# Kernel optimization log

Hardware: AMD Instinct MI355X
Metric: run time of the kernel (lower is better)

## Reference

```python
import jax, jax.numpy as jnp
import numpy as np

B, S, T = 32, 64, 64
E, H = 256, 512
VS, VT = 32000, 32000


def setup_inputs() -> dict:
    key = jax.random.key(0)
    ks = jax.random.split(key, 32)
    g = lambda i, shape: jax.random.normal(ks[i], shape, jnp.float32) * 0.05
    inp = {
        "src": jax.random.randint(ks[0], (B, S), 0, VS),
        "tgt": jax.random.randint(ks[1], (B, T), 0, VT),
        # encoder
        "enc_emb": g(2, (VS, E)),
        "enc_wih0": g(3, (3 * H, E)), "enc_whh0": g(4, (3 * H, H)),
        "enc_bih0": g(5, (3 * H,)), "enc_bhh0": g(6, (3 * H,)),
        "enc_wih1": g(7, (3 * H, H)), "enc_whh1": g(8, (3 * H, H)),
        "enc_bih1": g(9, (3 * H,)), "enc_bhh1": g(10, (3 * H,)),
        # decoder (layer0 input = embed + encoder context = E + H)
        "dec_emb": g(11, (VT, E)),
        "dec_wih0": g(12, (3 * H, E + H)), "dec_whh0": g(13, (3 * H, H)),
        "dec_bih0": g(14, (3 * H,)), "dec_bhh0": g(15, (3 * H,)),
        "dec_wih1": g(16, (3 * H, H)), "dec_whh1": g(17, (3 * H, H)),
        "dec_bih1": g(18, (3 * H,)), "dec_bhh1": g(19, (3 * H,)),
        # general (Luong) attention: score = q W_a k^T
        "attn_w": g(20, (H, H)),
        # output projection: Linear(hidden + enc_hidden -> tgt_vocab)
        "out_w": g(21, (VT, 2 * H)), "out_b": g(22, (VT,)),
    }
    return inp


def _gru_step(x, h, wih, whh, bih, bhh):
    # torch GRU cell math
    gi = x @ wih.T + bih
    gh = h @ whh.T + bhh
    i_r, i_z, i_n = jnp.split(gi, 3, axis=-1)
    h_r, h_z, h_n = jnp.split(gh, 3, axis=-1)
    r = jax.nn.sigmoid(i_r + h_r)
    z = jax.nn.sigmoid(i_z + h_z)
    n = jnp.tanh(i_n + r * h_n)
    return (1.0 - z) * n + z * h


def reference(src, tgt, enc_emb, enc_wih0, enc_whh0, enc_bih0, enc_bhh0,
              enc_wih1, enc_whh1, enc_bih1, enc_bhh1,
              dec_emb, dec_wih0, dec_whh0, dec_bih0, dec_bhh0,
              dec_wih1, dec_whh1, dec_bih1, dec_bhh1,
              attn_w, out_w, out_b):
    b = src.shape[0]
    h = enc_whh0.shape[1]
    # ---- encoder: 2-layer GRU over src ----
    xs = jnp.swapaxes(enc_emb[src], 0, 1)  # [S, B, E]
    h0 = jnp.zeros((b, h), jnp.float32)
    h1 = jnp.zeros((b, h), jnp.float32)

    def enc_step(carry, x_t):
        c0, c1 = carry
        c0 = _gru_step(x_t, c0, enc_wih0, enc_whh0, enc_bih0, enc_bhh0)
        c1 = _gru_step(c0, c1, enc_wih1, enc_whh1, enc_bih1, enc_bhh1)
        return (c0, c1), c1

    (h0, h1), enc_seq = jax.lax.scan(enc_step, (h0, h1), xs)
    enc_out = jnp.swapaxes(enc_seq, 0, 1)  # [B, S, H]
    mask = src == 0  # pad positions

    # ---- decoder: teacher forcing (ratio=1.0) over tgt[:, :-1] ----
    ctx0 = jnp.zeros((b, h), jnp.float32)
    toks = jnp.swapaxes(tgt[:, :-1], 0, 1)  # [T-1, B]

    def dec_step(carry, tok):
        d0, d1, ctx = carry
        emb = dec_emb[tok]  # [B, E]
        rin = jnp.concatenate([emb, ctx], axis=-1)
        d0 = _gru_step(rin, d0, dec_wih0, dec_whh0, dec_bih0, dec_bhh0)
        d1 = _gru_step(d0, d1, dec_wih1, dec_whh1, dec_bih1, dec_bhh1)
        # general attention: score = (q W_a) . k
        scores = jnp.einsum('bh,hk,bsk->bs', d1, attn_w, enc_out)
        scores = jnp.where(mask, -1e9, scores)
        w = jax.nn.softmax(scores, axis=-1)
        new_ctx = jnp.einsum('bs,bsh->bh', w, enc_out)
        logits = jnp.concatenate([d1, new_ctx], axis=-1) @ out_w.T + out_b
        return (d0, d1, new_ctx), logits

    _, logits = jax.lax.scan(dec_step, (h0, h1, ctx0), toks)
    return jnp.swapaxes(logits, 0, 1)  # [B, T-1, VT]
```

## Files before the change

kernel.cpp:

```cpp
#include <hip/hip_runtime.h>

#define Bz   32
#define Sz   64
#define Tdec 63
#define Ez   256
#define Hz   512
#define H3z  1536
#define Vz   32000
#define NB   128

typedef __attribute__((ext_vector_type(4))) float f32x4;
typedef __attribute__((ext_vector_type(4))) float floatx4;
typedef __attribute__((ext_vector_type(8))) short shortx8;
typedef __attribute__((ext_vector_type(8))) unsigned short u16x8;

__device__ __forceinline__ unsigned short f2bf(float f) {
  unsigned x = __float_as_uint(f);
  unsigned r = (x + 0x7fffu + ((x >> 16) & 1u)) >> 16;
  return (unsigned short)r;
}

__device__ __forceinline__ f32x4 ld_sc_nw(const f32x4* p) {
  f32x4 r;
  asm volatile("global_load_dwordx4 %0, %1, off sc0 sc1" : "=&v"(r) : "v"(p));
  return r;
}
__device__ __forceinline__ void wait_vm0() {
  asm volatile("s_waitcnt vmcnt(0)" ::: "memory");
}
__device__ __forceinline__ void ld2f_sc(const float* p0, const float* p1,
                                        float& a, float& b) {
  asm volatile(
      "global_load_dword %0, %2, off sc0 sc1\n\t"
      "global_load_dword %1, %3, off sc0 sc1\n\t"
      "s_waitcnt vmcnt(0)"
      : "=&v"(a), "=&v"(b) : "v"(p0), "v"(p1) : "memory");
}
__device__ __forceinline__ void st_sc(float* p, float v) {
  asm volatile("global_store_dword %0, %1, off sc0 sc1" :: "v"(p), "v"(v) : "memory");
}
__device__ __forceinline__ void st_flag(unsigned* p, unsigned v) {
  asm volatile("global_store_dword %0, %1, off sc0 sc1" :: "v"(p), "v"(v) : "memory");
}
__device__ __forceinline__ void ld2u_sc(const unsigned* p0, const unsigned* p1,
                                        unsigned& a, unsigned& b) {
  asm volatile(
      "global_load_dword %0, %2, off sc0 sc1\n\t"
      "global_load_dword %1, %3, off sc0 sc1\n\t"
      "s_waitcnt vmcnt(0)"
      : "=&v"(a), "=&v"(b) : "v"(p0), "v"(p1) : "memory");
}

__global__ __launch_bounds__(256)
void k_transpose(const float* __restrict__ in, int R, int Ctot, int c0,
                 float* __restrict__ out) {
  __shared__ float tile[32][33];
  int ct = blockIdx.x * 32;
  int rt = blockIdx.y * 32;
  int lx = threadIdx.x & 31, ly = threadIdx.x >> 5;
#pragma unroll
  for (int i = 0; i < 32; i += 8)
    tile[ly + i][lx] = in[(long)(rt + ly + i) * Ctot + c0 + ct + lx];
  __syncthreads();
#pragma unroll
  for (int i = 0; i < 32; i += 8)
    out[(long)(ct + ly + i) * R + rt + lx] = tile[lx][ly + i];
}

__global__ __launch_bounds__(256)
void k_pack4(const float* __restrict__ in, int rs, int c0,
             float* __restrict__ out, int k4off) {
  int jl = threadIdx.x & 15, k4l = threadIdx.x >> 4;
  int j = blockIdx.y * 16 + jl;
  int k4 = blockIdx.x * 16 + k4l;
  float4 v = *(const float4*)(in + (long)j * rs + c0 + k4 * 4);
  *(float4*)(out + ((long)(k4 + k4off) * H3z + j) * 4) = v;
}

__global__ __launch_bounds__(256)
void k_packbf(const float* __restrict__ in, int rs, int c0,
              unsigned short* __restrict__ out, int k8off) {
  int jl = threadIdx.x & 31, k8l = threadIdx.x >> 5;
  int j = blockIdx.y * 32 + jl;
  int k8 = blockIdx.x * 8 + k8l;
  const float* src = in + (long)j * rs + c0 + k8 * 8;
  float4 a = *(const float4*)src;
  float4 b = *(const float4*)(src + 4);
  u16x8 o;
  o[0] = f2bf(a.x); o[1] = f2bf(a.y); o[2] = f2bf(a.z); o[3] = f2bf(a.w);
  o[4] = f2bf(b.x); o[5] = f2bf(b.y); o[6] = f2bf(b.z); o[7] = f2bf(b.w);
  *(u16x8*)(out + ((long)(k8 + k8off) * H3z + j) * 8) = o;
}

__global__ __launch_bounds__(256)
void k_embed_gi(const int* __restrict__ toks, const float* __restrict__ emb,
                const float* __restrict__ W4, const float* __restrict__ bias,
                float* __restrict__ G) {
  __shared__ float se[16][Ez];
  int jg = blockIdx.x % 24;
  int rg = blockIdx.x / 24;
  int r0 = rg * 16;
  int tid = threadIdx.x;
  for (int c = tid; c < 16 * Ez; c += 256) {
    int rl = c >> 8;
    int k = c & 255;
    int r = r0 + rl;
    int tok = toks[(r & 31) * 64 + (r >> 5)];
    se[rl][k] = emb[(long)tok * Ez + k];
  }
  __syncthreads();
  int jj = tid & 63, rq = tid >> 6;
  int j = jg * 64 + jj;
  float a0 = 0.f, a1 = 0.f, a2 = 0.f, a3 = 0.f;
#pragma unroll 4
  for (int k4 = 0; k4 < 64; ++k4) {
    float4 w = *(const float4*)(W4 + ((long)k4 * H3z + j) * 4);
    const float* s0 = &se[rq * 4 + 0][k4 * 4];
    const float* s1 = &se[rq * 4 + 1][k4 * 4];
    const float* s2 = &se[rq * 4 + 2][k4 * 4];
    const float* s3 = &se[rq * 4 + 3][k4 * 4];
    a0 = fmaf(s0[3], w.w, fmaf(s0[2], w.z, fmaf(s0[1], w.y, fmaf(s0[0], w.x, a0))));
    a1 = fmaf(s1[3], w.w, fmaf(s1[2], w.z, fmaf(s1[1], w.y, fmaf(s1[0], w.x, a1))));
    a2 = fmaf(s2[3], w.w, fmaf(s2[2], w.z, fmaf(s2[1], w.y, fmaf(s2[0], w.x, a2))));
    a3 = fmaf(s3[3], w.w, fmaf(s3[2], w.z, fmaf(s3[1], w.y, fmaf(s3[0], w.x, a3))));
  }
  float bj = bias[j];
  G[(long)(r0 + rq * 4 + 0) * H3z + j] = a0 + bj;
  G[(long)(r0 + rq * 4 + 1) * H3z + j] = a1 + bj;
  G[(long)(r0 + rq * 4 + 2) * H3z + j] = a2 + bj;
  G[(long)(r0 + rq * 4 + 3) * H3z + j] = a3 + bj;
}

__global__ void k_f2bf(const float* __restrict__ in, unsigned short* __restrict__ out, long n4) {
  long i = (long)blockIdx.x * blockDim.x + threadIdx.x;
  long stride = (long)gridDim.x * blockDim.x;
  for (; i < n4; i += stride) {
    float4 v = ((const float4*)in)[i];
    ushort4 o;
    o.x = f2bf(v.x); o.y = f2bf(v.y); o.z = f2bf(v.z); o.w = f2bf(v.w);
    ((ushort4*)out)[i] = o;
  }
}

struct PP {
  const float* giEnc;
  const float* giDec;
  const unsigned short* W8e0;
  const unsigned short* W8e1;
  const unsigned short* W8d0;
  const unsigned short* W8d1;
  const float* enc_bhh0;
  const float* enc_bih1;
  const float* enc_bhh1;
  const float* dec_bhh0;
  const float* dec_bih1;
  const float* dec_bhh1;
  const float* wtAttn;
  const int* src;
  float* h0; float* h1; float* d0; float* d1; float* ctx;
  float* encOut;
  float* encN;
  float* keN;
  unsigned* flags;
  unsigned short* d1ctxBf;
};

__device__ __forceinline__ void gsync(unsigned* flags, unsigned ph) {
  wait_vm0();
  __syncthreads();
  int tid = threadIdx.x;
  if (tid == 0) st_flag(&flags[blockIdx.x], ph);
  if (tid < 64) {
    const unsigned* p0 = &flags[tid];
    const unsigned* p1 = &flags[tid + 64];
    for (;;) {
      unsigned f0, f1;
      ld2u_sc(p0, p1, f0, f1);
      if (!__any(f0 < ph || f1 < ph)) break;
      __builtin_amdgcn_s_sleep(1);
    }
  }
  __syncthreads();
}

template <int HASX>
__device__ __forceinline__ void gru_cell(
    int blkid, const unsigned short* __restrict__ W8,
    const float* __restrict__ gi, const float* __restrict__ bih,
    const float* __restrict__ bhh,
    const float* __restrict__ xin, const float* __restrict__ hin,
    float* __restrict__ hout, float* __restrict__ fout, long fstride,
    unsigned short* __restrict__ bfout, float* smem) {
  float* sh = smem;
  float* sx = smem + 2048;
  float* part = smem + 4096;
  const int jg = blkid & 7, bg = blkid >> 3;
  const int tid = threadIdx.x;
  const int l = tid & 63;
  const int kq = tid >> 6;
  const int j = jg * 64 + l;
  constexpr int Q8 = HASX ? 32 : 16;
  constexpr int G8 = Q8 / 2;
  const u16x8* Wr0 = (const u16x8*)W8 + (long)(kq * Q8) * H3z + j;

  u16x8 wA[2][3], wB[2][3];
  {
    const u16x8* Wr = Wr0;
    wA[0][0] = Wr[0];    wA[0][1] = Wr[512];  wA[0][2] = Wr[1024];
    wA[1][0] = Wr[1536]; wA[1][1] = Wr[2048]; wA[1][2] = Wr[2560];
  }
  float gir = 0.f, giz = 0.f, gin = 0.f;
  {
    const int b4 = tid >> 6, jc = tid & 63;
    const int b = bg * 4 + b4, jj = jg * 64 + jc;
    if (gi) {
      gir = gi[(long)b * H3z + jj];
      giz = gi[(long)b * H3z + 512 + jj];
      gin = gi[(long)b * H3z + 1024 + jj];
    }
    if (bih) { gir += bih[jj]; giz += bih[512 + jj]; gin += bih[1024 + jj]; }
  }
  {
    const f32x4* hp = (const f32x4*)(hin + bg * 2048);
    if (HASX) {
      const f32x4* xp = (const f32x4*)(xin + bg * 2048);
      f32x4 a = ld_sc_nw(hp + tid);
      f32x4 b = ld_sc_nw(hp + tid + 256);
      f32x4 c = ld_sc_nw(xp + tid);
      f32x4 d = ld_sc_nw(xp + tid + 256);
      wait_vm0();
      ((f32x4*)sh)[tid] = a; ((f32x4*)sh)[tid + 256] = b;
      ((f32x4*)sx)[tid] = c; ((f32x4*)sx)[tid + 256] = d;
    } else {
      f32x4 a = ld_sc_nw(hp + tid);
      f32x4 b = ld_sc_nw(hp + tid + 256);
      wait_vm0();
      ((f32x4*)sh)[tid] = a; ((f32x4*)sh)[tid + 256] = b;
    }
  }
  __syncthreads();

  const float* vb;
  if (HASX) vb = (kq < 2) ? (sx + kq * 256) : (sh + (kq - 2) * 256);
  else      vb = sh + kq * 128;
  float pr[4] = {0, 0, 0, 0}, pz[4] = {0, 0, 0, 0}, pn[4] = {0, 0, 0, 0};

  auto loadg = [&](u16x8 (&w)[2][3], int g) {
    const u16x8* Wr = Wr0 + (long)(2 * g) * H3z;
    w[0][0] = Wr[0];    w[0][1] = Wr[512];  w[0][2] = Wr[1024];
    w[1][0] = Wr[1536]; w[1][1] = Wr[2048]; w[1][2] = Wr[2560];
  };
  auto compg = [&](u16x8 (&w)[2][3], int g) {
#pragma unroll
    for (int r = 0; r < 2; ++r) {
      const int kk = 2 * g + r;
      float f0[8], f1[8], f2[8];
#pragma unroll
      for (int e = 0; e < 8; ++e) {
        f0[e] = __uint_as_float((unsigned)w[r][0][e] << 16);
        f1[e] = __uint_as_float((unsigned)w[r][1][e] << 16);
        f2[e] = __uint_as_float((unsigned)w[r][2][e] << 16);
      }
#pragma unroll
      for (int b4 = 0; b4 < 4; ++b4) {
        const float* v = vb + kk * 8 + b4 * 512;
        f32x4 v0 = *(const f32x4*)v;
        f32x4 v1 = *(const f32x4*)(v + 4);
#pragma unroll
        for (int e = 0; e < 4; ++e) {
          pr[b4] = fmaf(v0[e], f0[e], pr[b4]);
          pz[b4] = fmaf(v0[e], f1[e], pz[b4]);
          pn[b4] = fmaf(v0[e], f2[e], pn[b4]);
        }
#pragma unroll
        for (int e = 0; e < 4; ++e) {
          pr[b4] = fmaf(v1[e], f0[4 + e], pr[b4]);
          pz[b4] = fmaf(v1[e], f1[4 + e], pz[b4]);
          pn[b4] = fmaf(v1[e], f2[4 + e], pn[b4]);
        }
      }
    }
  };
#pragma unroll
  for (int g = 0; g < G8; g += 2) {
    if (g + 1 < G8) loadg(wB, g + 1);
    compg(wA, g);
    if (g + 2 < G8) loadg(wA, g + 2);
    if (g + 1 < G8) compg(wB, g + 1);
  }

#pragma unroll
  for (int b4 = 0; b4 < 4; ++b4) {
    part[((0 * 4 + b4) * 4 + kq) * 64 + l] = pr[b4];
    part[((1 * 4 + b4) * 4 + kq) * 64 + l] = pz[b4];
    part[((2 * 4 + b4) * 4 + kq) * 64 + l] = pn[b4];
  }
  __syncthreads();
  {
    const int b4 = tid >> 6, jc = tid & 63;
    const int b = bg * 4 + b4;
    const int jj = jg * 64 + jc;
    float sr = 0.f, sz = 0.f, snx = 0.f, snh = 0.f;
#pragma unroll
    for (int q = 0; q < 4; ++q) {
      sr += part[((0 * 4 + b4) * 4 + q) * 64 + jc];
      sz += part[((1 * 4 + b4) * 4 + q) * 64 + jc];
      float pnq = part[((2 * 4 + b4) * 4 + q) * 64 + jc];
      if (HASX && q < 2) snx += pnq; else snh += pnq;
    }
    float rv = 1.f / (1.f + __expf(-(gir + sr + bhh[jj])));
    float zv = 1.f / (1.f + __expf(-(giz + sz + bhh[512 + jj])));
    float nv = tanhf(gin + snx + rv * (snh + bhh[1024 + jj]));
    float hv = sh[b4 * 512 + jj];
    float hp = (1.f - zv) * nv + zv * hv;
    st_sc(hout + (long)b * 512 + jj, hp);
    if (fout) st_sc(fout + (long)b * fstride + jj, hp);
    if (bfout) bfout[(long)b * 1024 + jj] = f2bf(hp);
  }
}

__device__ void ke_phase(int blk, const float* __restrict__ encOut,
                         const float* __restrict__ attn_wT,
                         float* __restrict__ keN, float* __restrict__ encN,
                         float* smem) {
  int b = blk & 31, sq = blk >> 5;
  long r0 = (long)b * 64 + sq * 16;
  int tid = threadIdx.x;
  {
    const f32x4* ep = (const f32x4*)(encOut + r0 * 512);
    f32x4 v[8];
#pragma unroll
    for (int u = 0; u < 8; ++u) v[u] = ld_sc_nw(ep + tid + u * 256);
    wait_vm0();
    f32x4* en = (f32x4*)(encN + r0 * 512);
#pragma unroll
    for (int u = 0; u < 8; ++u) {
      ((f32x4*)smem)[tid + u * 256] = v[u];
      en[tid + u * 256] = v[u];
    }
  }
  __syncthreads();
  int jj = tid & 63, rq = tid >> 6;
  float acc[4][8];
#pragma unroll
  for (int r = 0; r < 4; ++r)
#pragma unroll
    for (int jc = 0; jc < 8; ++jc) acc[r][jc] = 0.f;
#pragma unroll 2
  for (int k = 0; k < 512; ++k) {
    float w[8];
#pragma unroll
    for (int jc = 0; jc < 8; ++jc) w[jc] = attn_wT[(long)k * 512 + jc * 64 + jj];
#pragma unroll
    for (int r = 0; r < 4; ++r) {
      float e = smem[(rq * 4 + r) * 512 + k];
#pragma unroll
      for (int jc = 0; jc < 8; ++jc) acc[r][jc] = fmaf(e, w[jc], acc[r][jc]);
    }
  }
#pragma unroll
  for (int r = 0; r < 4; ++r)
#pragma unroll
    for (int jc = 0; jc < 8; ++jc)
      keN[(r0 + rq * 4 + r) * 512 + jc * 64 + jj] = acc[r][jc];
}

__device__ void attn_phase(int b, const float* __restrict__ d1,
                           const float* __restrict__ keN,
                           const float* __restrict__ encN,
                           const int* __restrict__ src,
                           float* __restrict__ ctxn,
                           unsigned short* __restrict__ bfctx, float* smem) {
  float* sd = smem;
  float* sc = smem + 512;
  int tid = threadIdx.x;
  {
    float a, c;
    ld2f_sc(d1 + b * 512 + tid, d1 + b * 512 + tid + 256, a, c);
    sd[tid] = a;
    sd[tid + 256] = c;
  }
  __syncthreads();
  int s = tid >> 2, q = tid & 3;
  const float4* kp = (const float4*)(keN + ((long)b * 64 + s) * 512 + q * 128);
  const float4* dp = (const float4*)(sd + q * 128);
  float p = 0.f;
#pragma unroll 8
  for (int i = 0; i < 32; ++i) {
    float4 v = kp[i];
    float4 d = dp[i];
    p += v.x * d.x + v.y * d.y + v.z * d.z + v.w * d.w;
  }
  p += __shfl_xor(p, 1);
  p += __shfl_xor(p, 2);
  if (q == 0) sc[s] = (src[b * 64 + s] == 0) ? -1e9f : p;
  __syncthreads();
  if (tid < 64) {
    float v = sc[tid];
    float m = v;
    for (int o = 32; o; o >>= 1) m = fmaxf(m, __shfl_xor(m, o));
    float e = __expf(v - m);
    float sum = e;
    for (int o = 32; o; o >>= 1) sum += __shfl_xor(sum, o);
    sc[tid] = e / sum;
  }
  __syncthreads();
  float a0 = 0.f, a1 = 0.f;
#pragma unroll 4
  for (int s2 = 0; s2 < 64; ++s2) {
    float w = sc[s2];
    const float* er = encN + ((long)b * 64 + s2) * 512;
    a0 = fmaf(w, er[tid], a0);
    a1 = fmaf(w, er[tid + 256], a1);
  }
  st_sc(ctxn + b * 512 + tid, a0);
  st_sc(ctxn + b * 512 + tid + 256, a1);
  bfctx[b * 1024 + tid] = f2bf(a0);
  bfctx[b * 1024 + tid + 256] = f2bf(a1);
}

__global__ __launch_bounds__(256) void k_persist(PP P) {
  __shared__ float smem[8192];
  int blk = blockIdx.x;
  unsigned ph = 0;
  for (int i = 0; i < Sz + 1; ++i) {
    if (i < Sz && blk < 64) {
      gru_cell<0>(blk, P.W8e0, P.giEnc + (long)i * 49152, nullptr, P.enc_bhh0,
                  nullptr, P.h0 + (i & 1) * 16384, P.h0 + ((i + 1) & 1) * 16384,
                  nullptr, 0, nullptr, smem);
    } else if (i >= 1 && blk >= 64) {
      int t = i - 1;
      gru_cell<1>(blk - 64, P.W8e1, nullptr, P.enc_bih1, P.enc_bhh1,
                  P.h0 + (i & 1) * 16384, P.h1 + (t & 1) * 16384,
                  P.h1 + ((t + 1) & 1) * 16384,
                  P.encOut + (long)t * 512, (long)Sz * 512, nullptr, smem);
    }
    gsync(P.flags, ++ph);
  }
  ke_phase(blk, P.encOut, P.wtAttn, P.keN, P.encN, smem);
  gsync(P.flags, ++ph);
  for (int t = 0; t < Tdec; ++t) {
    int cs = t & 1, ns = (t + 1) & 1;
    const float* d0in = (t == 0) ? P.h0 : P.d0 + cs * 16384;
    const float* d1in = (t == 0) ? P.h1 : P.d1 + cs * 16384;
    if (blk < 64) {
      gru_cell<1>(blk, P.W8d0, P.giDec + (long)t * 49152, nullptr, P.dec_bhh0,
                  P.ctx + cs * 16384, d0in, P.d0 + ns * 16384,
                  nullptr, 0, nullptr, smem);
    }
    gsync(P.flags, ++ph);
    if (blk < 64) {
      gru_cell<1>(blk, P.W8d1, nullptr, P.dec_bih1, P.dec_bhh1,
                  P.d0 + ns * 16384, d1in, P.d1 + ns * 16384,
                  nullptr, 0, P.d1ctxBf + (long)t * 32768, smem);
    }
    gsync(P.flags, ++ph);
    if (blk < 32) {
      attn_phase(blk, P.d1 + ns * 16384, P.keN, P.encN, P.src,
                 P.ctx + ns * 16384, P.d1ctxBf + (long)t * 32768 + 512, smem);
    }
    gsync(P.flags, ++ph);
  }
}

__global__ __launch_bounds__(256)
void k_out_gemm(const unsigned short* __restrict__ A, const unsigned short* __restrict__ Bw,
                const float* __restrict__ bias, float* __restrict__ out) {
  __shared__ __align__(16) char lds[32768];
  int bid = blockIdx.x;
  int bm = bid & 15, bn = bid >> 4;
  long m0 = (long)bm * 128, n0 = (long)bn * 128;
  int tid = threadIdx.x, lane = tid & 63, wid = tid >> 6;
  int wm = wid >> 1, wn = wid & 1;
  floatx4 acc[4][4];
#pragma unroll
  for (int i = 0; i < 4; i++)
#pragma unroll
    for (int jx = 0; jx < 4; jx++) acc[i][jx] = (floatx4){0.f, 0.f, 0.f, 0.f};

  int rl = lane >> 3;
  int kb = (((lane & 7) ^ rl) << 4);

  for (int kt = 0; kt < 16; ++kt) {
    long kbyte0 = (long)kt * 128;
#pragma unroll
    for (int q = 0; q < 4; ++q) {
      int c = wid * 4 + q;
      int row = c * 8 + rl;
      const char* ga = (const char*)A + (m0 + row) * 2048 + kbyte0 + kb;
      const char* gb = (const char*)Bw + (n0 + row) * 2048 + kbyte0 + kb;
      __builtin_amdgcn_global_load_lds(
          (const __attribute__((address_space(1))) void*)ga,
          (__attribute__((address_space(3))) void*)(lds + (c << 10)), 16, 0, 0);
      __builtin_amdgcn_global_load_lds(
          (const __attribute__((address_space(1))) void*)gb,
          (__attribute__((address_space(3))) void*)(lds + 16384 + (c << 10)), 16, 0, 0);
    }
    asm volatile("s_waitcnt vmcnt(0)" ::: "memory");
    __syncthreads();
#pragma unroll
    for (int kk = 0; kk < 2; ++kk) {
      shortx8 af[4], bf[4];
#pragma unroll
      for (int f = 0; f < 4; ++f) {
        int rowA = wm * 64 + f * 16 + (lane & 15);
        int cbA = (kk * 64 + ((lane >> 4) << 4)) ^ ((rowA & 7) << 4);
        af[f] = *(const shortx8*)(lds + rowA * 128 + cbA);
        int rowB = wn * 64 + f * 16 + (lane & 15);
        int cbB = (kk * 64 + ((lane >> 4) << 4)) ^ ((rowB & 7) << 4);
        bf[f] = *(const shortx8*)(lds + 16384 + rowB * 128 + cbB);
      }
#pragma unroll
      for (int mf = 0; mf < 4; ++mf)
#pragma unroll
        for (int nf = 0; nf < 4; ++nf)
          acc[mf][nf] = __builtin_amdgcn_mfma_f32_16x16x32_bf16(af[mf], bf[nf], acc[mf][nf], 0, 0, 0);
    }
    __syncthreads();
  }
#pragma unroll
  for (int mf = 0; mf < 4; ++mf) {
#pragma unroll
    for (int nf = 0; nf < 4; ++nf) {
      long gn = n0 + wn * 64 + nf * 16 + (lane & 15);
      float bb = bias[gn];
#pragma unroll
      for (int r = 0; r < 4; ++r) {
        long gm = m0 + wm * 64 + mf * 16 + ((lane >> 4) * 4) + r;
        if (gm < (long)Tdec * Bz) {
          long t = gm >> 5, b = gm & 31;
          out[(b * Tdec + t) * (long)Vz + gn] = acc[mf][nf][r] + bb;
        }
      }
    }
  }
}

extern "C" void kernel_launch(void* const* d_in, const int* in_sizes, int n_in,
                              void* d_out, int out_size, void* d_ws, size_t ws_size,
                              hipStream_t stream) {
  const int*   src      = (const int*)d_in[0];
  const int*   tgt      = (const int*)d_in[1];
  const float* enc_emb  = (const float*)d_in[2];
  const float* enc_wih0 = (const float*)d_in[3];
  const float* enc_whh0 = (const float*)d_in[4];
  const float* enc_bih0 = (const float*)d_in[5];
  const float* enc_bhh0 = (const float*)d_in[6];
  const float* enc_wih1 = (const float*)d_in[7];
  const float* enc_whh1 = (const float*)d_in[8];
  const float* enc_bih1 = (const float*)d_in[9];
  const float* enc_bhh1 = (const float*)d_in[10];
  const float* dec_emb  = (const float*)d_in[11];
  const float* dec_wih0 = (const float*)d_in[12];
  const float* dec_whh0 = (const float*)d_in[13];
  const float* dec_bih0 = (const float*)d_in[14];
  const float* dec_bhh0 = (const float*)d_in[15];
  const float* dec_wih1 = (const float*)d_in[16];
  const float* dec_whh1 = (const float*)d_in[17];
  const float* dec_bih1 = (const float*)d_in[18];
  const float* dec_bhh1 = (const float*)d_in[19];
  const float* attn_w   = (const float*)d_in[20];
  const float* out_w    = (const float*)d_in[21];
  const float* out_b    = (const float*)d_in[22];
  float* out = (float*)d_out;

  char* ws = (char*)d_ws;
  size_t off = 0;
  auto alloc = [&](size_t bytes) -> char* {
    char* p = ws + off;
    off += (bytes + 255) & ~(size_t)255;
    return p;
  };
  float* W4embE = (float*)alloc((size_t)Ez * H3z * 4);
  float* W4embD = (float*)alloc((size_t)Ez * H3z * 4);
  unsigned short* W8e0 = (unsigned short*)alloc((size_t)64 * H3z * 8 * 2);
  unsigned short* W8e1 = (unsigned short*)alloc((size_t)128 * H3z * 8 * 2);
  unsigned short* W8d0 = (unsigned short*)alloc((size_t)128 * H3z * 8 * 2);
  unsigned short* W8d1 = (unsigned short*)alloc((size_t)128 * H3z * 8 * 2);
  float* wtAttn = (float*)alloc((size_t)Hz * Hz * 4);
  float* giEnc  = (float*)alloc((size_t)Sz * Bz * H3z * 4);
  float* giDec  = (float*)alloc((size_t)Tdec * Bz * H3z * 4);
  float* encOut = (float*)alloc((size_t)Bz * Sz * Hz * 4);
  float* encN   = (float*)alloc((size_t)Bz * Sz * Hz * 4);
  float* keN    = (float*)alloc((size_t)Bz * Sz * Hz * 4);
  float* h0buf  = (float*)alloc((size_t)2 * Bz * Hz * 4);
  float* h1buf  = (float*)alloc((size_t)2 * Bz * Hz * 4);
  float* d0buf  = (float*)alloc((size_t)2 * Bz * Hz * 4);
  float* d1buf  = (float*)alloc((size_t)2 * Bz * Hz * 4);
  float* ctxbuf = (float*)alloc((size_t)2 * Bz * Hz * 4);
  unsigned short* d1ctxBf = (unsigned short*)alloc((size_t)2048 * 1024 * 2);
  unsigned short* outwBf  = (unsigned short*)alloc((size_t)Vz * 1024 * 2);
  unsigned* flags = (unsigned*)alloc(NB * 4);
  if (off > ws_size) return;

  dim3 tb(256);
  k_pack4<<<dim3(4, 96), tb, 0, stream>>>(enc_wih0, Ez, 0, W4embE, 0);
  k_pack4<<<dim3(4, 96), tb, 0, stream>>>(dec_wih0, Ez + Hz, 0, W4embD, 0);
  k_packbf<<<dim3(8, 48), tb, 0, stream>>>(enc_whh0, Hz, 0, W8e0, 0);
  k_packbf<<<dim3(8, 48), tb, 0, stream>>>(enc_wih1, Hz, 0, W8e1, 0);
  k_packbf<<<dim3(8, 48), tb, 0, stream>>>(enc_whh1, Hz, 0, W8e1, 64);
  k_packbf<<<dim3(8, 48), tb, 0, stream>>>(dec_wih0, Ez + Hz, Ez, W8d0, 0);
  k_packbf<<<dim3(8, 48), tb, 0, stream>>>(dec_whh0, Hz, 0, W8d0, 64);
  k_packbf<<<dim3(8, 48), tb, 0, stream>>>(dec_wih1, Hz, 0, W8d1, 0);
  k_packbf<<<dim3(8, 48), tb, 0, stream>>>(dec_whh1, Hz, 0, W8d1, 64);
  k_transpose<<<dim3(Hz / 32, Hz / 32), tb, 0, stream>>>(attn_w, Hz, Hz, 0, wtAttn);

  hipMemsetAsync(h0buf, 0, (size_t)2 * Bz * Hz * 4, stream);
  hipMemsetAsync(h1buf, 0, (size_t)2 * Bz * Hz * 4, stream);
  hipMemsetAsync(ctxbuf, 0, (size_t)2 * Bz * Hz * 4, stream);
  hipMemsetAsync(d1ctxBf + (size_t)2016 * 1024, 0, (size_t)32 * 1024 * 2, stream);
  hipMemsetAsync(flags, 0, NB * 4, stream);

  k_embed_gi<<<24 * 128, tb, 0, stream>>>(src, enc_emb, W4embE, enc_bih0, giEnc);
  k_embed_gi<<<24 * 126, tb, 0, stream>>>(tgt, dec_emb, W4embD, dec_bih0, giDec);
  k_f2bf<<<2048, tb, 0, stream>>>(out_w, outwBf, (long)Vz * 1024 / 4);

  PP pp;
  pp.giEnc = giEnc; pp.giDec = giDec;
  pp.W8e0 = W8e0; pp.W8e1 = W8e1; pp.W8d0 = W8d0; pp.W8d1 = W8d1;
  pp.enc_bhh0 = enc_bhh0; pp.enc_bih1 = enc_bih1; pp.enc_bhh1 = enc_bhh1;
  pp.dec_bhh0 = dec_bhh0; pp.dec_bih1 = dec_bih1; pp.dec_bhh1 = dec_bhh1;
  pp.wtAttn = wtAttn; pp.src = src;
  pp.h0 = h0buf; pp.h1 = h1buf; pp.d0 = d0buf; pp.d1 = d1buf; pp.ctx = ctxbuf;
  pp.encOut = encOut; pp.encN = encN; pp.keN = keN;
  pp.d1ctxBf = d1ctxBf; pp.flags = flags;
  k_persist<<<NB, tb, 0, stream>>>(pp);

  k_out_gemm<<<16 * 250, tb, 0, stream>>>(d1ctxBf, outwBf, out_b, out);
}
```

Baseline: 4.639 ms.

## Split decoder GRU into x/h parts across block halves, widen to 512 threads

```diff
diff --git a/kernel.cpp b/kernel.cpp
--- a/kernel.cpp
+++ b/kernel.cpp
@@ -19,6 +19,9 @@
   unsigned r = (x + 0x7fffu + ((x >> 16) & 1u)) >> 16;
   return (unsigned short)r;
 }
+__device__ __forceinline__ float bf2f(unsigned short u) {
+  return __uint_as_float((unsigned)u << 16);
+}
 
 __device__ __forceinline__ f32x4 ld_sc_nw(const f32x4* p) {
   f32x4 r;
@@ -28,13 +31,23 @@
 __device__ __forceinline__ void wait_vm0() {
   asm volatile("s_waitcnt vmcnt(0)" ::: "memory");
 }
-__device__ __forceinline__ void ld2f_sc(const float* p0, const float* p1,
-                                        float& a, float& b) {
+__device__ __forceinline__ void ld1f_sc(const float* p, float& a) {
   asm volatile(
-      "global_load_dword %0, %2, off sc0 sc1\n\t"
-      "global_load_dword %1, %3, off sc0 sc1\n\t"
+      "global_load_dword %0, %1, off sc0 sc1\n\t"
       "s_waitcnt vmcnt(0)"
-      : "=&v"(a), "=&v"(b) : "v"(p0), "v"(p1) : "memory");
+      : "=&v"(a) : "v"(p) : "memory");
+}
+__device__ __forceinline__ void ld4f_sc(const float* p0, const float* p1,
+                                        const float* p2, const float* p3,
+                                        float& a, float& b, float& c, float& d) {
+  asm volatile(
+      "global_load_dword %0, %4, off sc0 sc1\n\t"
+      "global_load_dword %1, %5, off sc0 sc1\n\t"
+      "global_load_dword %2, %6, off sc0 sc1\n\t"
+      "global_load_dword %3, %7, off sc0 sc1\n\t"
+      "s_waitcnt vmcnt(0)"
+      : "=&v"(a), "=&v"(b), "=&v"(c), "=&v"(d)
+      : "v"(p0), "v"(p1), "v"(p2), "v"(p3) : "memory");
 }
 __device__ __forceinline__ void st_sc(float* p, float v) {
   asm volatile("global_store_dword %0, %1, off sc0 sc1" :: "v"(p), "v"(v) : "memory");
@@ -147,8 +160,10 @@
   const float* giDec;
   const unsigned short* W8e0;
   const unsigned short* W8e1;
-  const unsigned short* W8d0;
-  const unsigned short* W8d1;
+  const unsigned short* W8d0x;
+  const unsigned short* W8d0h;
+  const unsigned short* W8d1x;
+  const unsigned short* W8d1h;
   const float* enc_bhh0;
   const float* enc_bih1;
   const float* enc_bhh1;
@@ -158,9 +173,10 @@
   const float* wtAttn;
   const int* src;
   float* h0; float* h1; float* d0; float* d1; float* ctx;
+  float* hpd0; float* hpd1;
   float* encOut;
-  float* encN;
-  float* keN;
+  unsigned short* keNb;
+  unsigned short* encNb;
   unsigned* flags;
   unsigned short* d1ctxBf;
 };
@@ -183,34 +199,34 @@
   __syncthreads();
 }
 
+#define W_PREFETCH_G0(Wr0, wA)                                        \
+  { const u16x8* Wr = (Wr0);                                          \
+    wA[0][0] = Wr[0];    wA[0][1] = Wr[512];  wA[0][2] = Wr[1024];    \
+    wA[1][0] = Wr[1536]; wA[1][1] = Wr[2048]; wA[1][2] = Wr[2560]; }
+
 template <int HASX>
-__device__ __forceinline__ void gru_cell(
+__device__ __forceinline__ void gru_full(
     int blkid, const unsigned short* __restrict__ W8,
     const float* __restrict__ gi, const float* __restrict__ bih,
     const float* __restrict__ bhh,
     const float* __restrict__ xin, const float* __restrict__ hin,
     float* __restrict__ hout, float* __restrict__ fout, long fstride,
-    unsigned short* __restrict__ bfout, float* smem) {
+    float* smem) {
   float* sh = smem;
   float* sx = smem + 2048;
   float* part = smem + 4096;
   const int jg = blkid & 7, bg = blkid >> 3;
   const int tid = threadIdx.x;
-  const int l = tid & 63;
-  const int kq = tid >> 6;
+  const int l = tid & 63, kq = tid >> 6;
   const int j = jg * 64 + l;
-  constexpr int Q8 = HASX ? 32 : 16;
+  constexpr int Q8 = HASX ? 16 : 8;
   constexpr int G8 = Q8 / 2;
   const u16x8* Wr0 = (const u16x8*)W8 + (long)(kq * Q8) * H3z + j;
 
   u16x8 wA[2][3], wB[2][3];
-  {
-    const u16x8* Wr = Wr0;
-    wA[0][0] = Wr[0];    wA[0][1] = Wr[512];  wA[0][2] = Wr[1024];
-    wA[1][0] = Wr[1536]; wA[1][1] = Wr[2048]; wA[1][2] = Wr[2560];
-  }
+  W_PREFETCH_G0(Wr0, wA);
   float gir = 0.f, giz = 0.f, gin = 0.f;
-  {
+  if (tid < 256) {
     const int b4 = tid >> 6, jc = tid & 63;
     const int b = bg * 4 + b4, jj = jg * 64 + jc;
     if (gi) {
@@ -222,29 +238,23 @@
   }
   {
     const f32x4* hp = (const f32x4*)(hin + bg * 2048);
+    f32x4 a = ld_sc_nw(hp + tid);
     if (HASX) {
       const f32x4* xp = (const f32x4*)(xin + bg * 2048);
-      f32x4 a = ld_sc_nw(hp + tid);
-      f32x4 b = ld_sc_nw(hp + tid + 256);
       f32x4 c = ld_sc_nw(xp + tid);
-      f32x4 d = ld_sc_nw(xp + tid + 256);
       wait_vm0();
-      ((f32x4*)sh)[tid] = a; ((f32x4*)sh)[tid + 256] = b;
-      ((f32x4*)sx)[tid] = c; ((f32x4*)sx)[tid + 256] = d;
+      ((f32x4*)sh)[tid] = a;
+      ((f32x4*)sx)[tid] = c;
     } else {
-      f32x4 a = ld_sc_nw(hp + tid);
-      f32x4 b = ld_sc_nw(hp + tid + 256);
       wait_vm0();
-      ((f32x4*)sh)[tid] = a; ((f32x4*)sh)[tid + 256] = b;
-    }
-  }
-  __syncthreads();
-
+      ((f32x4*)sh)[tid] = a;
+    }
+  }
+  __syncthreads();
   const float* vb;
-  if (HASX) vb = (kq < 2) ? (sx + kq * 256) : (sh + (kq - 2) * 256);
-  else      vb = sh + kq * 128;
+  if (HASX) vb = (kq < 4) ? (sx + kq * 128) : (sh + (kq - 4) * 128);
+  else      vb = sh + kq * 64;
   float pr[4] = {0, 0, 0, 0}, pz[4] = {0, 0, 0, 0}, pn[4] = {0, 0, 0, 0};
-
   auto loadg = [&](u16x8 (&w)[2][3], int g) {
     const u16x8* Wr = Wr0 + (long)(2 * g) * H3z;
     w[0][0] = Wr[0];    w[0][1] = Wr[512];  w[0][2] = Wr[1024];
@@ -257,9 +267,7 @@
       float f0[8], f1[8], f2[8];
 #pragma unroll
       for (int e = 0; e < 8; ++e) {
-        f0[e] = __uint_as_float((unsigned)w[r][0][e] << 16);
-        f1[e] = __uint_as_float((unsigned)w[r][1][e] << 16);
-        f2[e] = __uint_as_float((unsigned)w[r][2][e] << 16);
+        f0[e] = bf2f(w[r][0][e]); f1[e] = bf2f(w[r][1][e]); f2[e] = bf2f(w[r][2][e]);
       }
 #pragma unroll
       for (int b4 = 0; b4 < 4; ++b4) {
@@ -288,62 +296,258 @@
     if (g + 2 < G8) loadg(wA, g + 2);
     if (g + 1 < G8) compg(wB, g + 1);
   }
-
 #pragma unroll
   for (int b4 = 0; b4 < 4; ++b4) {
-    part[((0 * 4 + b4) * 4 + kq) * 64 + l] = pr[b4];
-    part[((1 * 4 + b4) * 4 + kq) * 64 + l] = pz[b4];
-    part[((2 * 4 + b4) * 4 + kq) * 64 + l] = pn[b4];
-  }
-  __syncthreads();
-  {
+    part[((0 * 4 + b4) * 8 + kq) * 64 + l] = pr[b4];
+    part[((1 * 4 + b4) * 8 + kq) * 64 + l] = pz[b4];
+    part[((2 * 4 + b4) * 8 + kq) * 64 + l] = pn[b4];
+  }
+  __syncthreads();
+  if (tid < 256) {
     const int b4 = tid >> 6, jc = tid & 63;
     const int b = bg * 4 + b4;
     const int jj = jg * 64 + jc;
     float sr = 0.f, sz = 0.f, snx = 0.f, snh = 0.f;
 #pragma unroll
-    for (int q = 0; q < 4; ++q) {
-      sr += part[((0 * 4 + b4) * 4 + q) * 64 + jc];
-      sz += part[((1 * 4 + b4) * 4 + q) * 64 + jc];
-      float pnq = part[((2 * 4 + b4) * 4 + q) * 64 + jc];
-      if (HASX && q < 2) snx += pnq; else snh += pnq;
+    for (int q = 0; q < 8; ++q) {
+      sr += part[((0 * 4 + b4) * 8 + q) * 64 + jc];
+      sz += part[((1 * 4 + b4) * 8 + q) * 64 + jc];
+      float pnq = part[((2 * 4 + b4) * 8 + q) * 64 + jc];
+      if (HASX && q < 4) snx += pnq; else snh += pnq;
     }
     float rv = 1.f / (1.f + __expf(-(gir + sr + bhh[jj])));
     float zv = 1.f / (1.f + __expf(-(giz + sz + bhh[512 + jj])));
     float nv = tanhf(gin + snx + rv * (snh + bhh[1024 + jj]));
     float hv = sh[b4 * 512 + jj];
-    float hp = (1.f - zv) * nv + zv * hv;
-    st_sc(hout + (long)b * 512 + jj, hp);
-    if (fout) st_sc(fout + (long)b * fstride + jj, hp);
-    if (bfout) bfout[(long)b * 1024 + jj] = f2bf(hp);
+    float hp2 = (1.f - zv) * nv + zv * hv;
+    st_sc(hout + (long)b * 512 + jj, hp2);
+    if (fout) st_sc(fout + (long)b * fstride + jj, hp2);
+  }
+}
+
+__device__ __forceinline__ void gru_xpart(
+    int blkid, const unsigned short* __restrict__ Wx,
+    const float* __restrict__ gi, const float* __restrict__ bih,
+    const float* __restrict__ bhh,
+    const float* __restrict__ xin, const float* __restrict__ hprev,
+    const float* __restrict__ hp, float* __restrict__ hout,
+    unsigned short* __restrict__ bfout, float* smem) {
+  float* sx = smem;
+  float* part = smem + 4096;
+  const int jg = blkid & 7, bg = blkid >> 3;
+  const int tid = threadIdx.x;
+  const int l = tid & 63, kq = tid >> 6;
+  const int j = jg * 64 + l;
+  const u16x8* Wr0 = (const u16x8*)Wx + (long)(kq * 8) * H3z + j;
+  u16x8 wA[2][3], wB[2][3];
+  W_PREFETCH_G0(Wr0, wA);
+  float gir = 0.f, giz = 0.f, gin = 0.f;
+  if (tid < 256) {
+    const int b4 = tid >> 6, jc = tid & 63;
+    const int b = bg * 4 + b4, jj = jg * 64 + jc;
+    if (gi) {
+      gir = gi[(long)b * H3z + jj];
+      giz = gi[(long)b * H3z + 512 + jj];
+      gin = gi[(long)b * H3z + 1024 + jj];
+    }
+    if (bih) { gir += bih[jj]; giz += bih[512 + jj]; gin += bih[1024 + jj]; }
+  }
+  {
+    const f32x4* xp = (const f32x4*)(xin + bg * 2048);
+    f32x4 a = ld_sc_nw(xp + tid);
+    wait_vm0();
+    ((f32x4*)sx)[tid] = a;
+  }
+  __syncthreads();
+  const float* vb = sx + kq * 64;
+  float pr[4] = {0, 0, 0, 0}, pz[4] = {0, 0, 0, 0}, pn[4] = {0, 0, 0, 0};
+  auto loadg = [&](u16x8 (&w)[2][3], int g) {
+    const u16x8* Wr = Wr0 + (long)(2 * g) * H3z;
+    w[0][0] = Wr[0];    w[0][1] = Wr[512];  w[0][2] = Wr[1024];
+    w[1][0] = Wr[1536]; w[1][1] = Wr[2048]; w[1][2] = Wr[2560];
+  };
+  auto compg = [&](u16x8 (&w)[2][3], int g) {
+#pragma unroll
+    for (int r = 0; r < 2; ++r) {
+      const int kk = 2 * g + r;
+      float f0[8], f1[8], f2[8];
+#pragma unroll
+      for (int e = 0; e < 8; ++e) {
+        f0[e] = bf2f(w[r][0][e]); f1[e] = bf2f(w[r][1][e]); f2[e] = bf2f(w[r][2][e]);
+      }
+#pragma unroll
+      for (int b4 = 0; b4 < 4; ++b4) {
+        const float* v = vb + kk * 8 + b4 * 512;
+        f32x4 v0 = *(const f32x4*)v;
+        f32x4 v1 = *(const f32x4*)(v + 4);
+#pragma unroll
+        for (int e = 0; e < 4; ++e) {
+          pr[b4] = fmaf(v0[e], f0[e], pr[b4]);
+          pz[b4] = fmaf(v0[e], f1[e], pz[b4]);
+          pn[b4] = fmaf(v0[e], f2[e], pn[b4]);
+        }
+#pragma unroll
+        for (int e = 0; e < 4; ++e) {
+          pr[b4] = fmaf(v1[e], f0[4 + e], pr[b4]);
+          pz[b4] = fmaf(v1[e], f1[4 + e], pz[b4]);
+          pn[b4] = fmaf(v1[e], f2[4 + e], pn[b4]);
+        }
+      }
+    }
+  };
+#pragma unroll
+  for (int g = 0; g < 4; g += 2) {
+    loadg(wB, g + 1);
+    compg(wA, g);
+    if (g + 2 < 4) loadg(wA, g + 2);
+    compg(wB, g + 1);
+  }
+#pragma unroll
+  for (int b4 = 0; b4 < 4; ++b4) {
+    part[((0 * 4 + b4) * 8 + kq) * 64 + l] = pr[b4];
+    part[((1 * 4 + b4) * 8 + kq) * 64 + l] = pz[b4];
+    part[((2 * 4 + b4) * 8 + kq) * 64 + l] = pn[b4];
+  }
+  __syncthreads();
+  if (tid < 256) {
+    const int b4 = tid >> 6, jc = tid & 63;
+    const int b = bg * 4 + b4;
+    const int jj = jg * 64 + jc;
+    float hr, hz, hn, hv;
+    ld4f_sc(hp + (long)(0 * 32 + b) * 512 + jj, hp + (long)(1 * 32 + b) * 512 + jj,
+            hp + (long)(2 * 32 + b) * 512 + jj, hprev + (long)b * 512 + jj,
+            hr, hz, hn, hv);
+    float sr = 0.f, sz = 0.f, sn = 0.f;
+#pragma unroll
+    for (int q = 0; q < 8; ++q) {
+      sr += part[((0 * 4 + b4) * 8 + q) * 64 + jc];
+      sz += part[((1 * 4 + b4) * 8 + q) * 64 + jc];
+      sn += part[((2 * 4 + b4) * 8 + q) * 64 + jc];
+    }
+    float rv = 1.f / (1.f + __expf(-(gir + sr + hr + bhh[jj])));
+    float zv = 1.f / (1.f + __expf(-(giz + sz + hz + bhh[512 + jj])));
+    float nv = tanhf(gin + sn + rv * (hn + bhh[1024 + jj]));
+    float hp2 = (1.f - zv) * nv + zv * hv;
+    st_sc(hout + (long)b * 512 + jj, hp2);
+    if (bfout) bfout[(long)b * 1024 + jj] = f2bf(hp2);
+  }
+}
+
+__device__ __forceinline__ void gru_hpart(
+    int blkid, const unsigned short* __restrict__ Wh,
+    const float* __restrict__ hin, float* __restrict__ hpOut, float* smem) {
+  float* sh = smem;
+  float* part = smem + 4096;
+  const int jg = blkid & 7, bg = blkid >> 3;
+  const int tid = threadIdx.x;
+  const int l = tid & 63, kq = tid >> 6;
+  const int j = jg * 64 + l;
+  const u16x8* Wr0 = (const u16x8*)Wh + (long)(kq * 8) * H3z + j;
+  u16x8 wA[2][3], wB[2][3];
+  W_PREFETCH_G0(Wr0, wA);
+  {
+    const f32x4* hp = (const f32x4*)(hin + bg * 2048);
+    f32x4 a = ld_sc_nw(hp + tid);
+    wait_vm0();
+    ((f32x4*)sh)[tid] = a;
+  }
+  __syncthreads();
+  const float* vb = sh + kq * 64;
+  float pr[4] = {0, 0, 0, 0}, pz[4] = {0, 0, 0, 0}, pn[4] = {0, 0, 0, 0};
+  auto loadg = [&](u16x8 (&w)[2][3], int g) {
+    const u16x8* Wr = Wr0 + (long)(2 * g) * H3z;
+    w[0][0] = Wr[0];    w[0][1] = Wr[512];  w[0][2] = Wr[1024];
+    w[1][0] = Wr[1536]; w[1][1] = Wr[2048]; w[1][2] = Wr[2560];
+  };
+  auto compg = [&](u16x8 (&w)[2][3], int g) {
+#pragma unroll
+    for (int r = 0; r < 2; ++r) {
+      const int kk = 2 * g + r;
+      float f0[8], f1[8], f2[8];
+#pragma unroll
+      for (int e = 0; e < 8; ++e) {
+        f0[e] = bf2f(w[r][0][e]); f1[e] = bf2f(w[r][1][e]); f2[e] = bf2f(w[r][2][e]);
+      }
+#pragma unroll
+      for (int b4 = 0; b4 < 4; ++b4) {
+        const float* v = vb + kk * 8 + b4 * 512;
+        f32x4 v0 = *(const f32x4*)v;
+        f32x4 v1 = *(const f32x4*)(v + 4);
+#pragma unroll
+        for (int e = 0; e < 4; ++e) {
+          pr[b4] = fmaf(v0[e], f0[e], pr[b4]);
+          pz[b4] = fmaf(v0[e], f1[e], pz[b4]);
+          pn[b4] = fmaf(v0[e], f2[e], pn[b4]);
+        }
+#pragma unroll
+        for (int e = 0; e < 4; ++e) {
+          pr[b4] = fmaf(v1[e], f0[4 + e], pr[b4]);
+          pz[b4] = fmaf(v1[e], f1[4 + e], pz[b4]);
+          pn[b4] = fmaf(v1[e], f2[4 + e], pn[b4]);
+        }
+      }
+    }
+  };
+#pragma unroll
+  for (int g = 0; g < 4; g += 2) {
+    loadg(wB, g + 1);
+    compg(wA, g);
+    if (g + 2 < 4) loadg(wA, g + 2);
+    compg(wB, g + 1);
+  }
+#pragma unroll
+  for (int b4 = 0; b4 < 4; ++b4) {
+    part[((0 * 4 + b4) * 8 + kq) * 64 + l] = pr[b4];
+    part[((1 * 4 + b4) * 8 + kq) * 64 + l] = pz[b4];
+    part[((2 * 4 + b4) * 8 + kq) * 64 + l] = pn[b4];
+  }
+  __syncthreads();
+  if (tid < 256) {
+    const int b4 = tid >> 6, jc = tid & 63;
+    const int b = bg * 4 + b4;
+    const int jj = jg * 64 + jc;
+    float s0 = 0.f, s1 = 0.f, s2 = 0.f;
+#pragma unroll
+    for (int q = 0; q < 8; ++q) {
+      s0 += part[((0 * 4 + b4) * 8 + q) * 64 + jc];
+      s1 += part[((1 * 4 + b4) * 8 + q) * 64 + jc];
+      s2 += part[((2 * 4 + b4) * 8 + q) * 64 + jc];
+    }
+    st_sc(hpOut + (long)(0 * 32 + b) * 512 + jj, s0);
+    st_sc(hpOut + (long)(1 * 32 + b) * 512 + jj, s1);
+    st_sc(hpOut + (long)(2 * 32 + b) * 512 + jj, s2);
   }
 }
 
 __device__ void ke_phase(int blk, const float* __restrict__ encOut,
                          const float* __restrict__ attn_wT,
-                         float* __restrict__ keN, float* __restrict__ encN,
-                         float* smem) {
+                         unsigned short* __restrict__ keNb,
+                         unsigned short* __restrict__ encNb, float* smem) {
   int b = blk & 31, sq = blk >> 5;
   long r0 = (long)b * 64 + sq * 16;
   int tid = threadIdx.x;
   {
     const f32x4* ep = (const f32x4*)(encOut + r0 * 512);
-    f32x4 v[8];
-#pragma unroll
-    for (int u = 0; u < 8; ++u) v[u] = ld_sc_nw(ep + tid + u * 256);
+    f32x4 v[4];
+#pragma unroll
+    for (int u = 0; u < 4; ++u) v[u] = ld_sc_nw(ep + tid + u * 512);
     wait_vm0();
-    f32x4* en = (f32x4*)(encN + r0 * 512);
-#pragma unroll
-    for (int u = 0; u < 8; ++u) {
-      ((f32x4*)smem)[tid + u * 256] = v[u];
-      en[tid + u * 256] = v[u];
-    }
-  }
-  __syncthreads();
+#pragma unroll
+    for (int u = 0; u < 4; ++u) ((f32x4*)smem)[tid + u * 512] = v[u];
+  }
+  __syncthreads();
+  {
+    u16x8 o0, o1;
+    const float* s = smem + tid * 16;
+#pragma unroll
+    for (int e = 0; e < 8; ++e) { o0[e] = f2bf(s[e]); o1[e] = f2bf(s[8 + e]); }
+    *(u16x8*)(encNb + r0 * 512 + tid * 16) = o0;
+    *(u16x8*)(encNb + r0 * 512 + tid * 16 + 8) = o1;
+  }
   int jj = tid & 63, rq = tid >> 6;
-  float acc[4][8];
-#pragma unroll
-  for (int r = 0; r < 4; ++r)
+  float acc[2][8];
+#pragma unroll
+  for (int r = 0; r < 2; ++r)
 #pragma unroll
     for (int jc = 0; jc < 8; ++jc) acc[r][jc] = 0.f;
 #pragma unroll 2
@@ -351,23 +555,23 @@
     float w[8];
 #pragma unroll
     for (int jc = 0; jc < 8; ++jc) w[jc] = attn_wT[(long)k * 512 + jc * 64 + jj];
-#pragma unroll
-    for (int r = 0; r < 4; ++r) {
-      float e = smem[(rq * 4 + r) * 512 + k];
-#pragma unroll
-      for (int jc = 0; jc < 8; ++jc) acc[r][jc] = fmaf(e, w[jc], acc[r][jc]);
-    }
-  }
-#pragma unroll
-  for (int r = 0; r < 4; ++r)
+    float e0 = smem[(rq * 2) * 512 + k], e1 = smem[(rq * 2 + 1) * 512 + k];
+#pragma unroll
+    for (int jc = 0; jc < 8; ++jc) {
+      acc[0][jc] = fmaf(e0, w[jc], acc[0][jc]);
+      acc[1][jc] = fmaf(e1, w[jc], acc[1][jc]);
+    }
+  }
+#pragma unroll
+  for (int r = 0; r < 2; ++r)
 #pragma unroll
     for (int jc = 0; jc < 8; ++jc)
-      keN[(r0 + rq * 4 + r) * 512 + jc * 64 + jj] = acc[r][jc];
+      keNb[(r0 + rq * 2 + r) * 512 + jc * 64 + jj] = f2bf(acc[r][jc]);
 }
 
 __device__ void attn_phase(int b, const float* __restrict__ d1,
-                           const float* __restrict__ keN,
-                           const float* __restrict__ encN,
+                           const unsigned short* __restrict__ keNb,
+                           const unsigned short* __restrict__ encNb,
                            const int* __restrict__ src,
                            float* __restrict__ ctxn,
                            unsigned short* __restrict__ bfctx, float* smem) {
@@ -375,24 +579,24 @@
   float* sc = smem + 512;
   int tid = threadIdx.x;
   {
-    float a, c;
-    ld2f_sc(d1 + b * 512 + tid, d1 + b * 512 + tid + 256, a, c);
+    float a;
+    ld1f_sc(d1 + b * 512 + tid, a);
     sd[tid] = a;
-    sd[tid + 256] = c;
-  }
-  __syncthreads();
-  int s = tid >> 2, q = tid & 3;
-  const float4* kp = (const float4*)(keN + ((long)b * 64 + s) * 512 + q * 128);
-  const float4* dp = (const float4*)(sd + q * 128);
+  }
+  __syncthreads();
+  int s = tid >> 3, q = tid & 7;
+  const u16x8* kp = (const u16x8*)(keNb + ((long)b * 64 + s) * 512 + q * 64);
+  const float* dp = sd + q * 64;
   float p = 0.f;
-#pragma unroll 8
-  for (int i = 0; i < 32; ++i) {
-    float4 v = kp[i];
-    float4 d = dp[i];
-    p += v.x * d.x + v.y * d.y + v.z * d.z + v.w * d.w;
+#pragma unroll
+  for (int e = 0; e < 8; ++e) {
+    u16x8 kv = kp[e];
+#pragma unroll
+    for (int i = 0; i < 8; ++i) p = fmaf(bf2f(kv[i]), dp[e * 8 + i], p);
   }
   p += __shfl_xor(p, 1);
   p += __shfl_xor(p, 2);
+  p += __shfl_xor(p, 4);
   if (q == 0) sc[s] = (src[b * 64 + s] == 0) ? -1e9f : p;
   __syncthreads();
   if (tid < 64) {
@@ -405,60 +609,58 @@
     sc[tid] = e / sum;
   }
   __syncthreads();
-  float a0 = 0.f, a1 = 0.f;
-#pragma unroll 4
-  for (int s2 = 0; s2 < 64; ++s2) {
-    float w = sc[s2];
-    const float* er = encN + ((long)b * 64 + s2) * 512;
-    a0 = fmaf(w, er[tid], a0);
-    a1 = fmaf(w, er[tid + 256], a1);
-  }
+  float a0 = 0.f;
+  const unsigned short* er = encNb + (long)b * 64 * 512 + tid;
+#pragma unroll 8
+  for (int s2 = 0; s2 < 64; ++s2) a0 = fmaf(sc[s2], bf2f(er[(long)s2 * 512]), a0);
   st_sc(ctxn + b * 512 + tid, a0);
-  st_sc(ctxn + b * 512 + tid + 256, a1);
   bfctx[b * 1024 + tid] = f2bf(a0);
-  bfctx[b * 1024 + tid + 256] = f2bf(a1);
-}
-
-__global__ __launch_bounds__(256) void k_persist(PP P) {
-  __shared__ float smem[8192];
+}
+
+__global__ __launch_bounds__(512, 2) void k_persist(PP P) {
+  __shared__ float smem[10240];
   int blk = blockIdx.x;
   unsigned ph = 0;
   for (int i = 0; i < Sz + 1; ++i) {
-    if (i < Sz && blk < 64) {
-      gru_cell<0>(blk, P.W8e0, P.giEnc + (long)i * 49152, nullptr, P.enc_bhh0,
-                  nullptr, P.h0 + (i & 1) * 16384, P.h0 + ((i + 1) & 1) * 16384,
-                  nullptr, 0, nullptr, smem);
-    } else if (i >= 1 && blk >= 64) {
+    if (blk < 64) {
+      if (i < Sz)
+        gru_full<0>(blk, P.W8e0, P.giEnc + (long)i * 49152, nullptr, P.enc_bhh0,
+                    nullptr, P.h0 + (i & 1) * 16384, P.h0 + ((i + 1) & 1) * 16384,
+                    nullptr, 0, smem);
+    } else if (i >= 1) {
       int t = i - 1;
-      gru_cell<1>(blk - 64, P.W8e1, nullptr, P.enc_bih1, P.enc_bhh1,
+      gru_full<1>(blk - 64, P.W8e1, nullptr, P.enc_bih1, P.enc_bhh1,
                   P.h0 + (i & 1) * 16384, P.h1 + (t & 1) * 16384,
                   P.h1 + ((t + 1) & 1) * 16384,
-                  P.encOut + (long)t * 512, (long)Sz * 512, nullptr, smem);
+                  P.encOut + (long)t * 512, (long)Sz * 512, smem);
     }
     gsync(P.flags, ++ph);
   }
-  ke_phase(blk, P.encOut, P.wtAttn, P.keN, P.encN, smem);
+  ke_phase(blk, P.encOut, P.wtAttn, P.keNb, P.encNb, smem);
+  gsync(P.flags, ++ph);
+  if (blk < 64) gru_hpart(blk, P.W8d0h, P.h0, P.hpd0, smem);
   gsync(P.flags, ++ph);
   for (int t = 0; t < Tdec; ++t) {
-    int cs = t & 1, ns = (t + 1) & 1;
-    const float* d0in = (t == 0) ? P.h0 : P.d0 + cs * 16384;
-    const float* d1in = (t == 0) ? P.h1 : P.d1 + cs * 16384;
-    if (blk < 64) {
-      gru_cell<1>(blk, P.W8d0, P.giDec + (long)t * 49152, nullptr, P.dec_bhh0,
-                  P.ctx + cs * 16384, d0in, P.d0 + ns * 16384,
-                  nullptr, 0, nullptr, smem);
-    }
+    int cs = t & 1, ps = cs ^ 1;
+    const float* d0prev = (t == 0) ? P.h0 : P.d0 + ps * 16384;
+    const float* d1prev = (t == 0) ? P.h1 : P.d1 + ps * 16384;
+    if (blk < 64)
+      gru_xpart(blk, P.W8d0x, P.giDec + (long)t * 49152, nullptr, P.dec_bhh0,
+                P.ctx + ps * 16384, d0prev, P.hpd0 + cs * 49152,
+                P.d0 + cs * 16384, nullptr, smem);
+    else
+      gru_hpart(blk - 64, P.W8d1h, d1prev, P.hpd1 + cs * 49152, smem);
     gsync(P.flags, ++ph);
-    if (blk < 64) {
-      gru_cell<1>(blk, P.W8d1, nullptr, P.dec_bih1, P.dec_bhh1,
-                  P.d0 + ns * 16384, d1in, P.d1 + ns * 16384,
-                  nullptr, 0, P.d1ctxBf + (long)t * 32768, smem);
-    }
+    if (blk < 64)
+      gru_xpart(blk, P.W8d1x, nullptr, P.dec_bih1, P.dec_bhh1,
+                P.d0 + cs * 16384, d1prev, P.hpd1 + cs * 49152,
+                P.d1 + cs * 16384, P.d1ctxBf + (long)t * 32768, smem);
+    else
+      gru_hpart(blk - 64, P.W8d0h, P.d0 + cs * 16384, P.hpd0 + ps * 49152, smem);
     gsync(P.flags, ++ph);
-    if (blk < 32) {
-      attn_phase(blk, P.d1 + ns * 16384, P.keN, P.encN, P.src,
-                 P.ctx + ns * 16384, P.d1ctxBf + (long)t * 32768 + 512, smem);
-    }
+    if (blk < 32)
+      attn_phase(blk, P.d1 + cs * 16384, P.keNb, P.encNb, P.src,
+                 P.ctx + cs * 16384, P.d1ctxBf + (long)t * 32768 + 512, smem);
     gsync(P.flags, ++ph);
   }
 }
@@ -573,21 +775,25 @@
   };
   float* W4embE = (float*)alloc((size_t)Ez * H3z * 4);
   float* W4embD = (float*)alloc((size_t)Ez * H3z * 4);
-  unsigned short* W8e0 = (unsigned short*)alloc((size_t)64 * H3z * 8 * 2);
-  unsigned short* W8e1 = (unsigned short*)alloc((size_t)128 * H3z * 8 * 2);
-  unsigned short* W8d0 = (unsigned short*)alloc((size_t)128 * H3z * 8 * 2);
-  unsigned short* W8d1 = (unsigned short*)alloc((size_t)128 * H3z * 8 * 2);
+  unsigned short* W8e0  = (unsigned short*)alloc((size_t)64 * H3z * 8 * 2);
+  unsigned short* W8e1  = (unsigned short*)alloc((size_t)128 * H3z * 8 * 2);
+  unsigned short* W8d0x = (unsigned short*)alloc((size_t)64 * H3z * 8 * 2);
+  unsigned short* W8d0h = (unsigned short*)alloc((size_t)64 * H3z * 8 * 2);
+  unsigned short* W8d1x = (unsigned short*)alloc((size_t)64 * H3z * 8 * 2);
+  unsigned short* W8d1h = (unsigned short*)alloc((size_t)64 * H3z * 8 * 2);
   float* wtAttn = (float*)alloc((size_t)Hz * Hz * 4);
   float* giEnc  = (float*)alloc((size_t)Sz * Bz * H3z * 4);
   float* giDec  = (float*)alloc((size_t)Tdec * Bz * H3z * 4);
   float* encOut = (float*)alloc((size_t)Bz * Sz * Hz * 4);
-  float* encN   = (float*)alloc((size_t)Bz * Sz * Hz * 4);
-  float* keN    = (float*)alloc((size_t)Bz * Sz * Hz * 4);
+  unsigned short* keNb  = (unsigned short*)alloc((size_t)Bz * Sz * Hz * 2);
+  unsigned short* encNb = (unsigned short*)alloc((size_t)Bz * Sz * Hz * 2);
   float* h0buf  = (float*)alloc((size_t)2 * Bz * Hz * 4);
   float* h1buf  = (float*)alloc((size_t)2 * Bz * Hz * 4);
   float* d0buf  = (float*)alloc((size_t)2 * Bz * Hz * 4);
   float* d1buf  = (float*)alloc((size_t)2 * Bz * Hz * 4);
   float* ctxbuf = (float*)alloc((size_t)2 * Bz * Hz * 4);
+  float* hpd0   = (float*)alloc((size_t)2 * 3 * Bz * Hz * 4);
+  float* hpd1   = (float*)alloc((size_t)2 * 3 * Bz * Hz * 4);
   unsigned short* d1ctxBf = (unsigned short*)alloc((size_t)2048 * 1024 * 2);
   unsigned short* outwBf  = (unsigned short*)alloc((size_t)Vz * 1024 * 2);
   unsigned* flags = (unsigned*)alloc(NB * 4);
@@ -599,10 +805,10 @@
   k_packbf<<<dim3(8, 48), tb, 0, stream>>>(enc_whh0, Hz, 0, W8e0, 0);
   k_packbf<<<dim3(8, 48), tb, 0, stream>>>(enc_wih1, Hz, 0, W8e1, 0);
   k_packbf<<<dim3(8, 48), tb, 0, stream>>>(enc_whh1, Hz, 0, W8e1, 64);
-  k_packbf<<<dim3(8, 48), tb, 0, stream>>>(dec_wih0, Ez + Hz, Ez, W8d0, 0);
-  k_packbf<<<dim3(8, 48), tb, 0, stream>>>(dec_whh0, Hz, 0, W8d0, 64);
-  k_packbf<<<dim3(8, 48), tb, 0, stream>>>(dec_wih1, Hz, 0, W8d1, 0);
-  k_packbf<<<dim3(8, 48), tb, 0, stream>>>(dec_whh1, Hz, 0, W8d1, 64);
+  k_packbf<<<dim3(8, 48), tb, 0, stream>>>(dec_wih0, Ez + Hz, Ez, W8d0x, 0);
+  k_packbf<<<dim3(8, 48), tb, 0, stream>>>(dec_whh0, Hz, 0, W8d0h, 0);
+  k_packbf<<<dim3(8, 48), tb, 0, stream>>>(dec_wih1, Hz, 0, W8d1x, 0);
+  k_packbf<<<dim3(8, 48), tb, 0, stream>>>(dec_whh1, Hz, 0, W8d1h, 0);
   k_transpose<<<dim3(Hz / 32, Hz / 32), tb, 0, stream>>>(attn_w, Hz, Hz, 0, wtAttn);
 
   hipMemsetAsync(h0buf, 0, (size_t)2 * Bz * Hz * 4, stream);
@@ -617,14 +823,16 @@
 
   PP pp;
   pp.giEnc = giEnc; pp.giDec = giDec;
-  pp.W8e0 = W8e0; pp.W8e1 = W8e1; pp.W8d0 = W8d0; pp.W8d1 = W8d1;
+  pp.W8e0 = W8e0; pp.W8e1 = W8e1;
+  pp.W8d0x = W8d0x; pp.W8d0h = W8d0h; pp.W8d1x = W8d1x; pp.W8d1h = W8d1h;
   pp.enc_bhh0 = enc_bhh0; pp.enc_bih1 = enc_bih1; pp.enc_bhh1 = enc_bhh1;
   pp.dec_bhh0 = dec_bhh0; pp.dec_bih1 = dec_bih1; pp.dec_bhh1 = dec_bhh1;
   pp.wtAttn = wtAttn; pp.src = src;
   pp.h0 = h0buf; pp.h1 = h1buf; pp.d0 = d0buf; pp.d1 = d1buf; pp.ctx = ctxbuf;
-  pp.encOut = encOut; pp.encN = encN; pp.keN = keN;
-  pp.d1ctxBf = d1ctxBf; pp.flags = flags;
-  k_persist<<<NB, tb, 0, stream>>>(pp);
+  pp.hpd0 = hpd0; pp.hpd1 = hpd1;
+  pp.encOut = encOut; pp.keNb = keNb; pp.encNb = encNb;
+  pp.flags = flags; pp.d1ctxBf = d1ctxBf;
+  k_persist<<<NB, dim3(512), 0, stream>>>(pp);
 
   k_out_gemm<<<16 * 250, tb, 0, stream>>>(d1ctxBf, outwBf, out_b, out);
 }
```

New measurement: 4.378 ms. 5.6% less time.
